# Kernel optimization log

Measured on AMD Instinct MI355X. Metric: run time of the kernel, lower is better.

The kernel has to match this reference:

```python
import jax, jax.numpy as jnp
import numpy as np

# par: dt=0.05, tau_m=10.0 -> alpha = 1 - dt/tau_m; v_th = 2.0
ALPHA = 1.0 - 0.05 / 10.0
V_TH = 2.0


def setup_inputs() -> dict:
    key = jax.random.key(0)
    k1, k2 = jax.random.split(key)
    B, T, N = 128, 1000, 1024
    x = jax.random.normal(k1, (B, T, N), dtype=jnp.float32)
    # torch init: normal(mean=0, std=1/sqrt(N))
    w = jax.random.normal(k2, (N,), dtype=jnp.float32) * (1.0 / np.sqrt(N))
    return {"x": x, "w": w}


def reference(x, w):
    """Runs the NeuronClass.__call__ LIF step over all T timesteps.

    v_t = alpha * v_{t-1} + x_t @ w - v_th * stop_grad(z_{t-1})
    z_t = 1[v_t - v_th > 0]
    Returns (v_seq, z_seq), each [B, T].
    """
    B, T, N = x.shape
    # Precompute the input current for all timesteps (same math as per-step x_t @ w,
    # but a single large GEMM instead of T small GEMVs).
    drive = jnp.einsum('btn,n->bt', x, w)  # [B, T]

    def step(carry, i_t):
        v, z = carry
        v = ALPHA * v + i_t - V_TH * jax.lax.stop_gradient(z)
        z = (v - V_TH > 0).astype(v.dtype)
        return (v, z), (v, z)

    v0 = jnp.zeros((B,), dtype=x.dtype)
    z0 = jnp.zeros((B,), dtype=x.dtype)
    _, (v_seq, z_seq) = jax.lax.scan(step, (v0, z0), drive.T)  # scanned outputs [T, B]
    return v_seq.T, z_seq.T
```

## Files before the change

### kernel.cpp

```cpp
#include <hip/hip_runtime.h>


#define ALPHA 0.995f
#define V_TH 2.0f

constexpr int B = 128;
constexpr int T = 1000;
constexpr int N = 1024;
constexpr int TILE_T = 8;
constexpr int NTILES = T / TILE_T;
constexpr int ROWS_PER_TILE = TILE_T * B;

typedef float f32x4 __attribute__((ext_vector_type(4)));

__global__ __launch_bounds__(256) void lif_fused_kernel(
    const float* __restrict__ x, const float* __restrict__ w,
    float* __restrict__ out, float* __restrict__ drive_t,
    unsigned int* __restrict__ tile_cnt) {
    __shared__ float s_v[B][TILE_T + 1];
    __shared__ float s_z[B][TILE_T + 1];
    const int tid = threadIdx.x;

    if (blockIdx.x == 0) {
        float v = 0.0f, z = 0.0f;
        for (int g = 0; g < NTILES; ++g) {
            if (tid == 0) {
                while (__hip_atomic_load(&tile_cnt[g], __ATOMIC_RELAXED,
                                         __HIP_MEMORY_SCOPE_AGENT) <
                       (unsigned)ROWS_PER_TILE)
                    __builtin_amdgcn_s_sleep(8);
            }
            __syncthreads();

            const int t0 = g * TILE_T;
            if (tid < B) {
                float d[TILE_T];
#pragma unroll
                for (int j = 0; j < TILE_T; ++j)
                    d[j] = __hip_atomic_load(&drive_t[(t0 + j) * B + tid],
                                             __ATOMIC_RELAXED,
                                             __HIP_MEMORY_SCOPE_AGENT);
                float vv = v, zz = z;
#pragma unroll
                for (int j = 0; j < TILE_T; ++j) {
                    vv = ALPHA * vv + d[j] - V_TH * zz;
                    zz = (vv - V_TH > 0.0f) ? 1.0f : 0.0f;
                    s_v[tid][j] = vv;
                    s_z[tid][j] = zz;
                }
                v = vv; z = zz;
            }
            __syncthreads();

            {
                const int bb = tid >> 1;
                const int j4 = (tid & 1) * 4;
                f32x4 vq = { s_v[bb][j4], s_v[bb][j4 + 1],
                             s_v[bb][j4 + 2], s_v[bb][j4 + 3] };
                *(f32x4*)(out + (long long)bb * T + t0 + j4) = vq;
                f32x4 zq = { s_z[bb][j4], s_z[bb][j4 + 1],
                             s_z[bb][j4 + 2], s_z[bb][j4 + 3] };
                *(f32x4*)(out + (long long)(B + bb) * T + t0 + j4) = zq;
            }
            __syncthreads();
        }
        return;
    }

    const int lane = tid & 63;
    const int gwave = (blockIdx.x - 1) * 4 + (tid >> 6);
    const int base = gwave * 4;
    const int g  = base >> 10;
    const int rem = base & 1023;
    const int b  = rem >> 3;
    const int j0 = rem & 7;
    const int t0 = g * TILE_T + j0;

    const float* wp = w + lane * 4;
    const f32x4 w0 = *(const f32x4*)(wp);
    const f32x4 w1 = *(const f32x4*)(wp + 256);
    const f32x4 w2 = *(const f32x4*)(wp + 512);
    const f32x4 w3 = *(const f32x4*)(wp + 768);

    const float* xb = x + ((long long)b * T + t0) * N + lane * 4;

#pragma unroll
    for (int i = 0; i < 4; i += 2) {
        const f32x4* xr0 = (const f32x4*)(xb + (long long)i * N);
        const f32x4* xr1 = (const f32x4*)((const float*)xr0 + N);
        const f32x4 a0 = __builtin_nontemporal_load(xr0);
        const f32x4 a1 = __builtin_nontemporal_load(xr0 + 64);
        const f32x4 a2 = __builtin_nontemporal_load(xr0 + 128);
        const f32x4 a3 = __builtin_nontemporal_load(xr0 + 192);
        const f32x4 b0 = __builtin_nontemporal_load(xr1);
        const f32x4 b1 = __builtin_nontemporal_load(xr1 + 64);
        const f32x4 b2 = __builtin_nontemporal_load(xr1 + 128);
        const f32x4 b3 = __builtin_nontemporal_load(xr1 + 192);

        double s0 = (double)a0.x*w0.x + (double)a0.y*w0.y + (double)a0.z*w0.z + (double)a0.w*w0.w;
        double s1 = (double)a1.x*w1.x + (double)a1.y*w1.y + (double)a1.z*w1.z + (double)a1.w*w1.w;
        double s2 = (double)a2.x*w2.x + (double)a2.y*w2.y + (double)a2.z*w2.z + (double)a2.w*w2.w;
        double s3 = (double)a3.x*w3.x + (double)a3.y*w3.y + (double)a3.z*w3.z + (double)a3.w*w3.w;
        double t0_ = (double)b0.x*w0.x + (double)b0.y*w0.y + (double)b0.z*w0.z + (double)b0.w*w0.w;
        double t1_ = (double)b1.x*w1.x + (double)b1.y*w1.y + (double)b1.z*w1.z + (double)b1.w*w1.w;
        double t2_ = (double)b2.x*w2.x + (double)b2.y*w2.y + (double)b2.z*w2.z + (double)b2.w*w2.w;
        double t3_ = (double)b3.x*w3.x + (double)b3.y*w3.y + (double)b3.z*w3.z + (double)b3.w*w3.w;
        double accA = (s0 + s1) + (s2 + s3);
        double accB = (t0_ + t1_) + (t2_ + t3_);

#pragma unroll
        for (int off = 32; off >= 1; off >>= 1) {
            accA += __shfl_down(accA, off);
            accB += __shfl_down(accB, off);
        }

        if (lane == 0) {
            __hip_atomic_store(&drive_t[(t0 + i) * B + b], (float)accA,
                               __ATOMIC_RELAXED, __HIP_MEMORY_SCOPE_AGENT);
            __hip_atomic_store(&drive_t[(t0 + i + 1) * B + b], (float)accB,
                               __ATOMIC_RELAXED, __HIP_MEMORY_SCOPE_AGENT);
        }
    }

    __syncthreads();
    if (tid == 0)
        __hip_atomic_fetch_add(&tile_cnt[g], 16u, __ATOMIC_RELAXED,
                               __HIP_MEMORY_SCOPE_AGENT);
}

extern "C" void kernel_launch(void* const* d_in, const int* in_sizes, int n_in,
                              void* d_out, int out_size, void* d_ws, size_t ws_size,
                              hipStream_t stream) {
    const float* x = (const float*)d_in[0];
    const float* w = (const float*)d_in[1];
    float* out = (float*)d_out;
    float* drive_t = (float*)d_ws;
    unsigned int* tile_cnt =
        (unsigned int*)((char*)d_ws + 512 * 1024);

    hipMemsetAsync(tile_cnt, 0, NTILES * sizeof(unsigned int), stream);

    lif_fused_kernel<<<8001, 256, 0, stream>>>(x, w, out, drive_t, tile_cnt);
}
```

Measured before the change: 717.3 us.

## Enlarge time tiles and drop block-wide barriers in serial LIF scan block

Time tiles grow from 8 to 40 steps, so the consumer block waits on the counter far fewer times. Each of the 128 scan threads now polls the tile counter itself instead of one thread polling and then a __syncthreads. Each thread writes its own v/z rows directly as float4 stores, so the shared-memory staging and its barriers are gone. The producer mapping is rewritten with divisions for the new tile size. The trade-off is more waiting before the first tile is ready, plus more redundant polling traffic to the counter.

```diff
diff --git a/kernel.cpp b/kernel.cpp
--- a/kernel.cpp
+++ b/kernel.cpp
@@ -7,9 +7,10 @@
 constexpr int B = 128;
 constexpr int T = 1000;
 constexpr int N = 1024;
-constexpr int TILE_T = 8;
+constexpr int TILE_T = 40;
 constexpr int NTILES = T / TILE_T;
 constexpr int ROWS_PER_TILE = TILE_T * B;
+constexpr int BLOCKS_PER_TILE = ROWS_PER_TILE / 16;
 
 typedef float f32x4 __attribute__((ext_vector_type(4)));
 
@@ -17,63 +18,50 @@
     const float* __restrict__ x, const float* __restrict__ w,
     float* __restrict__ out, float* __restrict__ drive_t,
     unsigned int* __restrict__ tile_cnt) {
-    __shared__ float s_v[B][TILE_T + 1];
-    __shared__ float s_z[B][TILE_T + 1];
     const int tid = threadIdx.x;
 
     if (blockIdx.x == 0) {
+        if (tid >= B) return;
         float v = 0.0f, z = 0.0f;
         for (int g = 0; g < NTILES; ++g) {
-            if (tid == 0) {
-                while (__hip_atomic_load(&tile_cnt[g], __ATOMIC_RELAXED,
-                                         __HIP_MEMORY_SCOPE_AGENT) <
-                       (unsigned)ROWS_PER_TILE)
-                    __builtin_amdgcn_s_sleep(8);
-            }
-            __syncthreads();
+            while (__hip_atomic_load(&tile_cnt[g], __ATOMIC_RELAXED,
+                                     __HIP_MEMORY_SCOPE_AGENT) <
+                   (unsigned)ROWS_PER_TILE)
+                __builtin_amdgcn_s_sleep(2);
 
             const int t0 = g * TILE_T;
-            if (tid < B) {
-                float d[TILE_T];
+            float d[TILE_T];
 #pragma unroll
-                for (int j = 0; j < TILE_T; ++j)
-                    d[j] = __hip_atomic_load(&drive_t[(t0 + j) * B + tid],
-                                             __ATOMIC_RELAXED,
-                                             __HIP_MEMORY_SCOPE_AGENT);
-                float vv = v, zz = z;
+            for (int j = 0; j < TILE_T; ++j)
+                d[j] = __hip_atomic_load(&drive_t[(t0 + j) * B + tid],
+                                         __ATOMIC_RELAXED,
+                                         __HIP_MEMORY_SCOPE_AGENT);
+
+            float* vout = out + (long long)tid * T + t0;
+            float* zout = out + (long long)(B + tid) * T + t0;
 #pragma unroll
-                for (int j = 0; j < TILE_T; ++j) {
-                    vv = ALPHA * vv + d[j] - V_TH * zz;
-                    zz = (vv - V_TH > 0.0f) ? 1.0f : 0.0f;
-                    s_v[tid][j] = vv;
-                    s_z[tid][j] = zz;
+            for (int j4 = 0; j4 < TILE_T; j4 += 4) {
+                f32x4 vq, zq;
+#pragma unroll
+                for (int k = 0; k < 4; ++k) {
+                    v = ALPHA * v + d[j4 + k] - V_TH * z;
+                    z = (v - V_TH > 0.0f) ? 1.0f : 0.0f;
+                    vq[k] = v;
+                    zq[k] = z;
                 }
-                v = vv; z = zz;
+                *(f32x4*)(vout + j4) = vq;
+                *(f32x4*)(zout + j4) = zq;
             }
-            __syncthreads();
-
-            {
-                const int bb = tid >> 1;
-                const int j4 = (tid & 1) * 4;
-                f32x4 vq = { s_v[bb][j4], s_v[bb][j4 + 1],
-                             s_v[bb][j4 + 2], s_v[bb][j4 + 3] };
-                *(f32x4*)(out + (long long)bb * T + t0 + j4) = vq;
-                f32x4 zq = { s_z[bb][j4], s_z[bb][j4 + 1],
-                             s_z[bb][j4 + 2], s_z[bb][j4 + 3] };
-                *(f32x4*)(out + (long long)(B + bb) * T + t0 + j4) = zq;
-            }
-            __syncthreads();
         }
         return;
     }
 
     const int lane = tid & 63;
-    const int gwave = (blockIdx.x - 1) * 4 + (tid >> 6);
-    const int base = gwave * 4;
-    const int g  = base >> 10;
-    const int rem = base & 1023;
-    const int b  = rem >> 3;
-    const int j0 = rem & 7;
+    const int R = (blockIdx.x - 1) * 16 + ((tid >> 6) << 2);
+    const int g = R / ROWS_PER_TILE;
+    const int rin = R - g * ROWS_PER_TILE;
+    const int b = rin / TILE_T;
+    const int j0 = rin - b * TILE_T;
     const int t0 = g * TILE_T + j0;
 
     const float* wp = w + lane * 4;
```

Result: faster. 690.9 us (-3.7%).
